# Optimization experiments

Measured on AMD Instinct MI355X. Metric: run time of the kernel, lower is better.

The kernel has to match this reference:

```python
import jax, jax.numpy as jnp
import numpy as np

B, L, K, D = 8, 4096, 16, 128


def setup_inputs() -> dict:
    key = jax.random.key(0)
    k1, k2 = jax.random.split(key)
    frame = jax.random.normal(k1, (B, L, 4, 3), dtype=jnp.float32)  # [B,L,4,3]: row0=center, rows1-3=frame axes
    attr = jax.random.normal(k2, (B, L, D), dtype=jnp.float32)
    return {"frame": frame, "attr": attr}


def reference(frame, attr):
    Kmax = 16
    center = frame[:, :, 0]  # [B,L,3]
    # pairwise squared distances (no grad needed through topk selection)
    c_ng = jax.lax.stop_gradient(center)
    diff = c_ng[:, :, None, :] - c_ng[:, None, :, :]  # [B,L,L,3]
    distance_sq = jnp.sum(diff * diff, axis=-1)  # [B,L,L]
    # k nearest neighbors (smallest distance)
    _, nbr = jax.lax.top_k(-distance_sq, Kmax)  # [B,L,K] int32 indices
    # gather neighbor attributes: attr[b, nbr[b,l,k], :]
    gathered_attr = jax.vmap(lambda a, i: a[i])(attr, nbr)  # [B,L,K,D]
    # gather neighbor centers and project delta into local frame
    nbr_center = jax.vmap(lambda c, i: c[i])(center, nbr)  # [B,L,K,3]
    delta = nbr_center - center[:, :, None, :]  # [B,L,K,3]
    euclidian = jnp.einsum('blkc,blcr->blkr', delta, frame[:, :, 1:4])  # [B,L,K,3]
    return (euclidian, gathered_attr)
```

## Files before the change

### kernel.cpp

```cpp
#include <hip/hip_runtime.h>
#include <stdint.h>

typedef unsigned long long u64;
typedef float nfloat4 __attribute__((ext_vector_type(4)));

#define LQ   4096
#define BQ   8
#define KNB  16
#define TPB  512
#define QPB  64
#define BPB  (LQ / QPB)

__device__ __forceinline__ void ceu(uint32_t &a, uint32_t &b) {
    const uint32_t mn = a < b ? a : b;
    const uint32_t mx = a < b ? b : a;
    a = mn; b = mx;
}
__device__ __forceinline__ void ced(double &a, double &b) {
    const double mn = __builtin_fmin(a, b);
    const double mx = __builtin_fmax(a, b);
    a = mn; b = mx;
}
__device__ __forceinline__ float dist2(float mx, float my, float mz,
                                       float px, float py, float pz) {
    const float dx = __fsub_rn(mx, px);
    const float dy = __fsub_rn(my, py);
    const float dz = __fsub_rn(mz, pz);
    return __fadd_rn(__fadd_rn(__fmul_rn(dx, dx), __fmul_rn(dy, dy)),
                     __fmul_rn(dz, dz));
}


__global__ __launch_bounds__(TPB) void knn_fused_kernel(
    const float4* __restrict__ frame4,
    const float4* __restrict__ attr4,
    float* __restrict__ out_e,
    nfloat4* __restrict__ outg4)
{
    __shared__ float xs[LQ], ys[LQ], zs[LQ];
    __shared__ unsigned short surv[QPB][32];
    __shared__ int nbrs[QPB][KNB];

    const int b    = blockIdx.x >> 6;
    const int qblk = blockIdx.x & (BPB - 1);
    const int tid  = threadIdx.x;

    const float4* fb = frame4 + (size_t)b * LQ * 3;
    for (int j = tid; j < LQ; j += TPB) {
        const float4 v = fb[j * 3];
        xs[j] = v.x; ys[j] = v.y; zs[j] = v.z;
    }
    __syncthreads();

    const int qloc = tid >> 3;
    const int h    = tid & 7;
    const int l    = qblk * QPB + qloc;
    const float mx = xs[l], my = ys[l], mz = zs[l];

    uint32_t R[16];
#pragma unroll
    for (int i = 0; i < 16; ++i) R[i] = 0xFFFFFFFFu;

#pragma unroll 1
    for (int cc = 0; cc < 64; ++cc) {
        uint32_t K[8];
#pragma unroll
        for (int s = 0; s < 8; ++s) {
            const int j = cc * 64 + s * 8 + h;
            const float d = dist2(mx, my, mz, xs[j], ys[j], zs[j]);
            K[s] = (__float_as_uint(d) & 0xFFFFF000u) | (unsigned)j;
        }
        ceu(K[0],K[1]); ceu(K[2],K[3]); ceu(K[4],K[5]); ceu(K[6],K[7]);
        ceu(K[0],K[2]); ceu(K[1],K[3]); ceu(K[4],K[6]); ceu(K[5],K[7]);
        ceu(K[1],K[2]); ceu(K[5],K[6]);
        ceu(K[0],K[4]); ceu(K[1],K[5]); ceu(K[2],K[6]); ceu(K[3],K[7]);
        ceu(K[2],K[4]); ceu(K[3],K[5]);
        ceu(K[1],K[2]); ceu(K[3],K[4]); ceu(K[5],K[6]);
#pragma unroll
        for (int t = 0; t < 8; ++t) {
            const uint32_t x = R[8 + t], y = K[7 - t];
            R[8 + t] = x < y ? x : y;
        }
#pragma unroll
        for (int g = 8; g >= 1; g >>= 1)
#pragma unroll
            for (int i = 0; i < 16; ++i)
                if ((i & g) == 0) ceu(R[i], R[i + g]);
    }

    {
        uint32_t P[16];
#pragma unroll
        for (int i = 0; i < 16; ++i) P[i] = __shfl_xor(R[i], 1, 64);
        const bool lo = (h & 1) == 0;
#pragma unroll
        for (int i = 0; i < 16; ++i) {
            const uint32_t o = P[15 - i];
            R[i] = lo ? (R[i] < o ? R[i] : o) : (R[i] > o ? R[i] : o);
        }
#pragma unroll
        for (int g = 8; g >= 1; g >>= 1)
#pragma unroll
            for (int i = 0; i < 16; ++i)
                if ((i & g) == 0) ceu(R[i], R[i + g]);
    }
    {
        uint32_t P[16];
#pragma unroll
        for (int i = 0; i < 16; ++i) P[i] = __shfl_xor(R[i], 3, 64);
        const bool lo = (h & 2) == 0;
#pragma unroll
        for (int i = 0; i < 16; ++i) {
            const uint32_t o = P[15 - i];
            R[i] = lo ? (R[i] < o ? R[i] : o) : (R[i] > o ? R[i] : o);
        }
#pragma unroll
        for (int i = 0; i < 16; ++i) P[i] = __shfl_xor(R[i], 1, 64);
        const bool lo1 = (h & 1) == 0;
#pragma unroll
        for (int i = 0; i < 16; ++i) {
            const uint32_t o = P[i];
            R[i] = lo1 ? (R[i] < o ? R[i] : o) : (R[i] > o ? R[i] : o);
        }
#pragma unroll
        for (int g = 8; g >= 1; g >>= 1)
#pragma unroll
            for (int i = 0; i < 16; ++i)
                if ((i & g) == 0) ceu(R[i], R[i + g]);
    }
    {
        uint32_t P[16];
#pragma unroll
        for (int i = 0; i < 16; ++i) P[i] = __shfl_xor(R[i], 7, 64);
        const bool lo = (h & 4) == 0;
#pragma unroll
        for (int i = 0; i < 16; ++i) {
            const uint32_t o = P[15 - i];
            R[i] = lo ? (R[i] < o ? R[i] : o) : (R[i] > o ? R[i] : o);
        }
#pragma unroll
        for (int i = 0; i < 16; ++i) P[i] = __shfl_xor(R[i], 2, 64);
        const bool lo2 = (h & 2) == 0;
#pragma unroll
        for (int i = 0; i < 16; ++i) {
            const uint32_t o = P[i];
            R[i] = lo2 ? (R[i] < o ? R[i] : o) : (R[i] > o ? R[i] : o);
        }
#pragma unroll
        for (int i = 0; i < 16; ++i) P[i] = __shfl_xor(R[i], 1, 64);
        const bool lo1 = (h & 1) == 0;
#pragma unroll
        for (int i = 0; i < 16; ++i) {
            const uint32_t o = P[i];
            R[i] = lo1 ? (R[i] < o ? R[i] : o) : (R[i] > o ? R[i] : o);
        }
#pragma unroll
        for (int g = 8; g >= 1; g >>= 1)
#pragma unroll
            for (int i = 0; i < 16; ++i)
                if ((i & g) == 0) ceu(R[i], R[i + g]);
    }

    if (h < 2) {
#pragma unroll
        for (int i = 0; i < 16; ++i)
            surv[qloc][h * 16 + i] = (unsigned short)(R[i] & 0xFFFu);
    }

    double kd[4];
#pragma unroll
    for (int s = 0; s < 4; ++s) {
        const int j = surv[qloc][h * 4 + s];
        const float d = dist2(mx, my, mz, xs[j], ys[j], zs[j]);
        kd[s] = __builtin_bit_cast(double,
                 ((u64)__float_as_uint(d) << 12) | (unsigned)j);
    }
    ced(kd[0],kd[1]); ced(kd[2],kd[3]); ced(kd[0],kd[2]); ced(kd[1],kd[3]); ced(kd[1],kd[2]);
    {
        double P[4];
#pragma unroll
        for (int s = 0; s < 4; ++s) P[s] = __shfl_xor(kd[s], 1, 64);
        const bool lo = (h & 1) == 0;
#pragma unroll
        for (int s = 0; s < 4; ++s) {
            const double o = P[3 - s];
            kd[s] = lo ? __builtin_fmin(kd[s], o) : __builtin_fmax(kd[s], o);
        }
        ced(kd[0],kd[2]); ced(kd[1],kd[3]); ced(kd[0],kd[1]); ced(kd[2],kd[3]);
    }
    {
        double P[4];
#pragma unroll
        for (int s = 0; s < 4; ++s) P[s] = __shfl_xor(kd[s], 3, 64);
        const bool lo = (h & 2) == 0;
#pragma unroll
        for (int s = 0; s < 4; ++s) {
            const double o = P[3 - s];
            kd[s] = lo ? __builtin_fmin(kd[s], o) : __builtin_fmax(kd[s], o);
        }
#pragma unroll
        for (int s = 0; s < 4; ++s) P[s] = __shfl_xor(kd[s], 1, 64);
        const bool lo1 = (h & 1) == 0;
#pragma unroll
        for (int s = 0; s < 4; ++s) {
            const double o = P[s];
            kd[s] = lo1 ? __builtin_fmin(kd[s], o) : __builtin_fmax(kd[s], o);
        }
        ced(kd[0],kd[2]); ced(kd[1],kd[3]); ced(kd[0],kd[1]); ced(kd[2],kd[3]);
    }
    {
        double P[4];
#pragma unroll
        for (int s = 0; s < 4; ++s) P[s] = __shfl_xor(kd[s], 7, 64);
        const bool lo = (h & 4) == 0;
#pragma unroll
        for (int s = 0; s < 4; ++s) {
            const double o = P[3 - s];
            kd[s] = lo ? __builtin_fmin(kd[s], o) : __builtin_fmax(kd[s], o);
        }
#pragma unroll
        for (int s = 0; s < 4; ++s) P[s] = __shfl_xor(kd[s], 2, 64);
        const bool lo2 = (h & 2) == 0;
#pragma unroll
        for (int s = 0; s < 4; ++s) {
            const double o = P[s];
            kd[s] = lo2 ? __builtin_fmin(kd[s], o) : __builtin_fmax(kd[s], o);
        }
#pragma unroll
        for (int s = 0; s < 4; ++s) P[s] = __shfl_xor(kd[s], 1, 64);
        const bool lo1 = (h & 1) == 0;
#pragma unroll
        for (int s = 0; s < 4; ++s) {
            const double o = P[s];
            kd[s] = lo1 ? __builtin_fmin(kd[s], o) : __builtin_fmax(kd[s], o);
        }
        ced(kd[0],kd[2]); ced(kd[1],kd[3]); ced(kd[0],kd[1]); ced(kd[2],kd[3]);
    }

    const size_t gq = (size_t)b * LQ + l;
    if (h < 4) {
        const float4 f0 = fb[l * 3 + 0];
        const float4 f1 = fb[l * 3 + 1];
        const float4 f2 = fb[l * 3 + 2];
        const float R00 = f0.w, R01 = f1.x, R02 = f1.y;
        const float R10 = f1.z, R11 = f1.w, R12 = f2.x;
        const float R20 = f2.y, R21 = f2.z, R22 = f2.w;
        float e[12];
#pragma unroll
        for (int s = 0; s < 4; ++s) {
            const u64 bits = __builtin_bit_cast(u64, kd[s]);
            const int j = (int)(bits & 0xFFFu);
            nbrs[qloc][h * 4 + s] = j;
            const float dx = xs[j] - mx;
            const float dy = ys[j] - my;
            const float dz = zs[j] - mz;
            e[s * 3 + 0] = dx * R00 + dy * R10 + dz * R20;
            e[s * 3 + 1] = dx * R01 + dy * R11 + dz * R21;
            e[s * 3 + 2] = dx * R02 + dy * R12 + dz * R22;
        }
        float4* eo = (float4*)(out_e + gq * 48 + h * 12);
        float4 v0 = {e[0], e[1], e[2],  e[3]};
        float4 v1 = {e[4], e[5], e[6],  e[7]};
        float4 v2 = {e[8], e[9], e[10], e[11]};
        eo[0] = v0; eo[1] = v1; eo[2] = v2;
    }

    const float4* ab = attr4 + (((size_t)b) << 12) * 32;
    const int wv = tid >> 6, lane = tid & 63;
    const size_t obase = ((size_t)b * LQ + (size_t)qblk * QPB + (size_t)wv * 8) * 512;
#pragma unroll 4
    for (int it = 0; it < 64; ++it) {
        const int idx = it * 64 + lane;
        const int qw  = idx >> 9;
        const int r   = idx & 511;
        const int k   = r >> 5, d4 = r & 31;
        const int nb  = nbrs[wv * 8 + qw][k];
        const float4 v = ab[(size_t)nb * 32 + d4];
        nfloat4 nv = {v.x, v.y, v.z, v.w};
        __builtin_nontemporal_store(nv, &outg4[obase + idx]);
    }
}

extern "C" void kernel_launch(void* const* d_in, const int* in_sizes, int n_in,
                              void* d_out, int out_size, void* d_ws, size_t ws_size,
                              hipStream_t stream)
{
    const float* frame = (const float*)d_in[0];
    const float* attr  = (const float*)d_in[1];
    float* out = (float*)d_out;

    nfloat4* outg4 = (nfloat4*)(out + (size_t)BQ * LQ * KNB * 3);
    knn_fused_kernel<<<BQ * BPB, TPB, 0, stream>>>(
        (const float4*)frame, (const float4*)attr, out, outg4);
}
```

Measured before the change: 329.0 us.

## Sort points by x and prune KNN scan with x-distance early termination

```diff
diff --git a/kernel.cpp b/kernel.cpp
--- a/kernel.cpp
+++ b/kernel.cpp
@@ -2,6 +2,7 @@
 #include <stdint.h>
 
 typedef unsigned long long u64;
+typedef unsigned short u16;
 typedef float nfloat4 __attribute__((ext_vector_type(4)));
 
 #define LQ   4096
@@ -30,15 +31,55 @@
                      __fmul_rn(dz, dz));
 }
 
+__global__ __launch_bounds__(512) void sort_kernel(
+    const float4* __restrict__ frame4,
+    float* __restrict__ wx, float* __restrict__ wy,
+    float* __restrict__ wz, int* __restrict__ wperm)
+{
+    __shared__ u64 SK[LQ];
+    const int b   = blockIdx.x;
+    const int tid = threadIdx.x;
+    const float4* fb = frame4 + (size_t)b * LQ * 3;
+
+    for (int j = tid; j < LQ; j += 512) {
+        const uint32_t bits = __float_as_uint(fb[j * 3].x);
+        const uint32_t mk = (bits & 0x80000000u) ? ~bits : (bits | 0x80000000u);
+        SK[j] = ((u64)mk << 32) | (unsigned)j;
+    }
+    __syncthreads();
+    for (int k = 2; k <= LQ; k <<= 1) {
+        for (int g = k >> 1; g >= 1; g >>= 1) {
+            for (int t = tid; t < LQ / 2; t += 512) {
+                const int i  = ((t & ~(g - 1)) << 1) | (t & (g - 1));
+                const int j2 = i | g;
+                const bool up = ((i & k) == 0);
+                const u64 a = SK[i], c = SK[j2];
+                if ((a > c) == up) { SK[i] = c; SK[j2] = a; }
+            }
+            __syncthreads();
+        }
+    }
+    for (int p = tid; p < LQ; p += 512) {
+        const int orig = (int)(SK[p] & 0xFFFu);
+        const float4 v = fb[orig * 3];
+        const size_t o = (size_t)b * LQ + p;
+        wx[o] = v.x; wy[o] = v.y; wz[o] = v.z; wperm[o] = orig;
+    }
+}
+
 
 __global__ __launch_bounds__(TPB) void knn_fused_kernel(
     const float4* __restrict__ frame4,
     const float4* __restrict__ attr4,
+    const float* __restrict__ wx, const float* __restrict__ wy,
+    const float* __restrict__ wz, const int* __restrict__ wperm,
     float* __restrict__ out_e,
     nfloat4* __restrict__ outg4)
 {
     __shared__ float xs[LQ], ys[LQ], zs[LQ];
-    __shared__ unsigned short surv[QPB][32];
+    __shared__ u16 perm_lds[LQ];
+    __shared__ u16 inv_lds[LQ];
+    __shared__ u16 surv[QPB][32];
     __shared__ int nbrs[QPB][KNB];
 
     const int b    = blockIdx.x >> 6;
@@ -46,29 +87,63 @@
     const int tid  = threadIdx.x;
 
     const float4* fb = frame4 + (size_t)b * LQ * 3;
-    for (int j = tid; j < LQ; j += TPB) {
-        const float4 v = fb[j * 3];
-        xs[j] = v.x; ys[j] = v.y; zs[j] = v.z;
+    {
+        const float* bx = wx + (size_t)b * LQ;
+        const float* by = wy + (size_t)b * LQ;
+        const float* bz = wz + (size_t)b * LQ;
+        const int*   bp = wperm + (size_t)b * LQ;
+        for (int j = tid; j < LQ; j += TPB) {
+            xs[j] = bx[j]; ys[j] = by[j]; zs[j] = bz[j];
+            const int pm = bp[j];
+            perm_lds[j] = (u16)pm;
+            inv_lds[pm] = (u16)j;
+        }
     }
     __syncthreads();
 
     const int qloc = tid >> 3;
     const int h    = tid & 7;
+    const int wv   = tid >> 6;
     const int l    = qblk * QPB + qloc;
     const float mx = xs[l], my = ys[l], mz = zs[l];
+    const float xq_lo = xs[qblk * QPB + wv * 8];
+    const float xq_hi = xs[qblk * QPB + wv * 8 + 7];
 
     uint32_t R[16];
 #pragma unroll
     for (int i = 0; i < 16; ++i) R[i] = 0xFFFFFFFFu;
 
+    const int A = qblk * QPB;
+    int lo = A, hi = A;
+    bool doneR = false;
+    bool doneL = (lo <= 0);
+
 #pragma unroll 1
-    for (int cc = 0; cc < 64; ++cc) {
+    while (!(doneR && doneL)) {
+        int base;
+        {
+            bool goRight;
+            if (doneR) goRight = false;
+            else if (doneL) goRight = true;
+            else {
+                const float dR = __fsub_rn(xs[hi], xq_hi);
+                const float dL = __fsub_rn(xq_lo, xs[lo - 1]);
+                goRight = !(dR > dL);
+            }
+            if (goRight) { base = hi; hi += 64; }
+            else         { lo -= 64; base = lo; }
+        }
         uint32_t K[8];
 #pragma unroll
         for (int s = 0; s < 8; ++s) {
-            const int j = cc * 64 + s * 8 + h;
-            const float d = dist2(mx, my, mz, xs[j], ys[j], zs[j]);
-            K[s] = (__float_as_uint(d) & 0xFFFFF000u) | (unsigned)j;
+            const int pos = base + s * 8 + h;
+            const int pp  = pos < 0 ? 0 : pos;
+            const float dx = __fsub_rn(mx, xs[pp]);
+            const float dy = __fsub_rn(my, ys[pp]);
+            const float dz = __fsub_rn(mz, zs[pp]);
+            const float d  = __fmaf_rn(dz, dz, __fmaf_rn(dy, dy, __fmul_rn(dx, dx)));
+            const uint32_t key = (__float_as_uint(d) & 0xFFFFF000u) | (unsigned)pos;
+            K[s] = (pos >= 0) ? key : 0xFFFFFFFFu;
         }
         ceu(K[0],K[1]); ceu(K[2],K[3]); ceu(K[4],K[5]); ceu(K[6],K[7]);
         ceu(K[0],K[2]); ceu(K[1],K[3]); ceu(K[4],K[6]); ceu(K[5],K[7]);
@@ -86,17 +161,46 @@
 #pragma unroll
             for (int i = 0; i < 16; ++i)
                 if ((i & g) == 0) ceu(R[i], R[i + g]);
+
+        uint32_t ub = R[15] | 0xFFFu;
+        { uint32_t t;
+          t = __shfl_xor(ub, 1, 64); ub = ub < t ? ub : t;
+          t = __shfl_xor(ub, 2, 64); ub = ub < t ? ub : t;
+          t = __shfl_xor(ub, 4, 64); ub = ub < t ? ub : t; }
+        uint32_t ubb = (ub & 0xFFFFF000u) | 0xFFFu;
+        ubb = ubb >> 12;
+        ubb = (ubb << 12) | 0xFFFu;
+        ubb = (ubb > 0xFFFFFFEFu) ? 0xFFFFFFFFu : ubb + 16u;
+
+        if (!doneR) {
+            if (hi >= LQ) doneR = true;
+            else {
+                const float dxm = __fsub_rn(xs[hi], mx);
+                const bool st = (dxm > 0.f) &&
+                                (__float_as_uint(__fmul_rn(dxm, dxm)) > ubb);
+                if (__all(st)) doneR = true;
+            }
+        }
+        if (!doneL) {
+            if (lo <= 0) doneL = true;
+            else {
+                const float dxm = __fsub_rn(mx, xs[lo - 1]);
+                const bool st = (dxm > 0.f) &&
+                                (__float_as_uint(__fmul_rn(dxm, dxm)) > ubb);
+                if (__all(st)) doneL = true;
+            }
+        }
     }
 
     {
         uint32_t P[16];
 #pragma unroll
         for (int i = 0; i < 16; ++i) P[i] = __shfl_xor(R[i], 1, 64);
-        const bool lo = (h & 1) == 0;
+        const bool lo1 = (h & 1) == 0;
 #pragma unroll
         for (int i = 0; i < 16; ++i) {
             const uint32_t o = P[15 - i];
-            R[i] = lo ? (R[i] < o ? R[i] : o) : (R[i] > o ? R[i] : o);
+            R[i] = lo1 ? (R[i] < o ? R[i] : o) : (R[i] > o ? R[i] : o);
         }
 #pragma unroll
         for (int g = 8; g >= 1; g >>= 1)
@@ -108,11 +212,11 @@
         uint32_t P[16];
 #pragma unroll
         for (int i = 0; i < 16; ++i) P[i] = __shfl_xor(R[i], 3, 64);
-        const bool lo = (h & 2) == 0;
+        const bool lo2 = (h & 2) == 0;
 #pragma unroll
         for (int i = 0; i < 16; ++i) {
             const uint32_t o = P[15 - i];
-            R[i] = lo ? (R[i] < o ? R[i] : o) : (R[i] > o ? R[i] : o);
+            R[i] = lo2 ? (R[i] < o ? R[i] : o) : (R[i] > o ? R[i] : o);
         }
 #pragma unroll
         for (int i = 0; i < 16; ++i) P[i] = __shfl_xor(R[i], 1, 64);
@@ -132,11 +236,11 @@
         uint32_t P[16];
 #pragma unroll
         for (int i = 0; i < 16; ++i) P[i] = __shfl_xor(R[i], 7, 64);
-        const bool lo = (h & 4) == 0;
+        const bool lo4 = (h & 4) == 0;
 #pragma unroll
         for (int i = 0; i < 16; ++i) {
             const uint32_t o = P[15 - i];
-            R[i] = lo ? (R[i] < o ? R[i] : o) : (R[i] > o ? R[i] : o);
+            R[i] = lo4 ? (R[i] < o ? R[i] : o) : (R[i] > o ? R[i] : o);
         }
 #pragma unroll
         for (int i = 0; i < 16; ++i) P[i] = __shfl_xor(R[i], 2, 64);
@@ -164,27 +268,27 @@
     if (h < 2) {
 #pragma unroll
         for (int i = 0; i < 16; ++i)
-            surv[qloc][h * 16 + i] = (unsigned short)(R[i] & 0xFFFu);
+            surv[qloc][h * 16 + i] = (u16)(R[i] & 0xFFFu);
     }
 
     double kd[4];
 #pragma unroll
     for (int s = 0; s < 4; ++s) {
-        const int j = surv[qloc][h * 4 + s];
-        const float d = dist2(mx, my, mz, xs[j], ys[j], zs[j]);
+        const int sp = surv[qloc][h * 4 + s];
+        const float d = dist2(mx, my, mz, xs[sp], ys[sp], zs[sp]);
         kd[s] = __builtin_bit_cast(double,
-                 ((u64)__float_as_uint(d) << 12) | (unsigned)j);
+                 ((u64)__float_as_uint(d) << 12) | (unsigned)perm_lds[sp]);
     }
     ced(kd[0],kd[1]); ced(kd[2],kd[3]); ced(kd[0],kd[2]); ced(kd[1],kd[3]); ced(kd[1],kd[2]);
     {
         double P[4];
 #pragma unroll
         for (int s = 0; s < 4; ++s) P[s] = __shfl_xor(kd[s], 1, 64);
-        const bool lo = (h & 1) == 0;
+        const bool lo1 = (h & 1) == 0;
 #pragma unroll
         for (int s = 0; s < 4; ++s) {
             const double o = P[3 - s];
-            kd[s] = lo ? __builtin_fmin(kd[s], o) : __builtin_fmax(kd[s], o);
+            kd[s] = lo1 ? __builtin_fmin(kd[s], o) : __builtin_fmax(kd[s], o);
         }
         ced(kd[0],kd[2]); ced(kd[1],kd[3]); ced(kd[0],kd[1]); ced(kd[2],kd[3]);
     }
@@ -192,11 +296,11 @@
         double P[4];
 #pragma unroll
         for (int s = 0; s < 4; ++s) P[s] = __shfl_xor(kd[s], 3, 64);
-        const bool lo = (h & 2) == 0;
+        const bool lo2 = (h & 2) == 0;
 #pragma unroll
         for (int s = 0; s < 4; ++s) {
             const double o = P[3 - s];
-            kd[s] = lo ? __builtin_fmin(kd[s], o) : __builtin_fmax(kd[s], o);
+            kd[s] = lo2 ? __builtin_fmin(kd[s], o) : __builtin_fmax(kd[s], o);
         }
 #pragma unroll
         for (int s = 0; s < 4; ++s) P[s] = __shfl_xor(kd[s], 1, 64);
@@ -212,11 +316,11 @@
         double P[4];
 #pragma unroll
         for (int s = 0; s < 4; ++s) P[s] = __shfl_xor(kd[s], 7, 64);
-        const bool lo = (h & 4) == 0;
+        const bool lo4 = (h & 4) == 0;
 #pragma unroll
         for (int s = 0; s < 4; ++s) {
             const double o = P[3 - s];
-            kd[s] = lo ? __builtin_fmin(kd[s], o) : __builtin_fmax(kd[s], o);
+            kd[s] = lo4 ? __builtin_fmin(kd[s], o) : __builtin_fmax(kd[s], o);
         }
 #pragma unroll
         for (int s = 0; s < 4; ++s) P[s] = __shfl_xor(kd[s], 2, 64);
@@ -237,11 +341,12 @@
         ced(kd[0],kd[2]); ced(kd[1],kd[3]); ced(kd[0],kd[1]); ced(kd[2],kd[3]);
     }
 
-    const size_t gq = (size_t)b * LQ + l;
+    const int ql_orig = perm_lds[l];
+    const size_t gq = (size_t)b * LQ + (size_t)ql_orig;
     if (h < 4) {
-        const float4 f0 = fb[l * 3 + 0];
-        const float4 f1 = fb[l * 3 + 1];
-        const float4 f2 = fb[l * 3 + 2];
+        const float4 f0 = fb[ql_orig * 3 + 0];
+        const float4 f1 = fb[ql_orig * 3 + 1];
+        const float4 f2 = fb[ql_orig * 3 + 2];
         const float R00 = f0.w, R01 = f1.x, R02 = f1.y;
         const float R10 = f1.z, R11 = f1.w, R12 = f2.x;
         const float R20 = f2.y, R21 = f2.z, R22 = f2.w;
@@ -249,11 +354,12 @@
 #pragma unroll
         for (int s = 0; s < 4; ++s) {
             const u64 bits = __builtin_bit_cast(u64, kd[s]);
-            const int j = (int)(bits & 0xFFFu);
-            nbrs[qloc][h * 4 + s] = j;
-            const float dx = xs[j] - mx;
-            const float dy = ys[j] - my;
-            const float dz = zs[j] - mz;
+            const int jo = (int)(bits & 0xFFFu);
+            nbrs[qloc][h * 4 + s] = jo;
+            const int sp = inv_lds[jo];
+            const float dx = xs[sp] - mx;
+            const float dy = ys[sp] - my;
+            const float dz = zs[sp] - mz;
             e[s * 3 + 0] = dx * R00 + dy * R10 + dz * R20;
             e[s * 3 + 1] = dx * R01 + dy * R11 + dz * R21;
             e[s * 3 + 2] = dx * R02 + dy * R12 + dz * R22;
@@ -266,8 +372,8 @@
     }
 
     const float4* ab = attr4 + (((size_t)b) << 12) * 32;
-    const int wv = tid >> 6, lane = tid & 63;
-    const size_t obase = ((size_t)b * LQ + (size_t)qblk * QPB + (size_t)wv * 8) * 512;
+    const int lane = tid & 63;
+    const int qbase = qblk * QPB + wv * 8;
 #pragma unroll 4
     for (int it = 0; it < 64; ++it) {
         const int idx = it * 64 + lane;
@@ -275,9 +381,11 @@
         const int r   = idx & 511;
         const int k   = r >> 5, d4 = r & 31;
         const int nb  = nbrs[wv * 8 + qw][k];
+        const int qo  = perm_lds[qbase + qw];
         const float4 v = ab[(size_t)nb * 32 + d4];
         nfloat4 nv = {v.x, v.y, v.z, v.w};
-        __builtin_nontemporal_store(nv, &outg4[obase + idx]);
+        __builtin_nontemporal_store(nv,
+            &outg4[((size_t)b * LQ + (size_t)qo) * 512 + r]);
     }
 }
 
@@ -289,7 +397,15 @@
     const float* attr  = (const float*)d_in[1];
     float* out = (float*)d_out;
 
+    float* wxp = (float*)d_ws;
+    float* wyp = wxp + BQ * LQ;
+    float* wzp = wyp + BQ * LQ;
+    int*   wpp = (int*)(wzp + BQ * LQ);
+
+    sort_kernel<<<BQ, 512, 0, stream>>>((const float4*)frame, wxp, wyp, wzp, wpp);
+
     nfloat4* outg4 = (nfloat4*)(out + (size_t)BQ * LQ * KNB * 3);
     knn_fused_kernel<<<BQ * BPB, TPB, 0, stream>>>(
-        (const float4*)frame, (const float4*)attr, out, outg4);
-}
+        (const float4*)frame, (const float4*)attr, wxp, wyp, wzp, wpp,
+        out, outg4);
+}
```

Result: slower. 396.8 us (+20.6%).

## Replace per-thread bitonic top-k with shared-memory histogram threshold selection

Applied to the files above, without the earlier changes.

```diff
diff --git a/kernel.cpp b/kernel.cpp
--- a/kernel.cpp
+++ b/kernel.cpp
@@ -2,6 +2,8 @@
 #include <stdint.h>
 
 typedef unsigned long long u64;
+typedef unsigned short u16;
+typedef unsigned int u32;
 typedef float nfloat4 __attribute__((ext_vector_type(4)));
 
 #define LQ   4096
@@ -10,12 +12,10 @@
 #define TPB  512
 #define QPB  64
 #define BPB  (LQ / QPB)
-
-__device__ __forceinline__ void ceu(uint32_t &a, uint32_t &b) {
-    const uint32_t mn = a < b ? a : b;
-    const uint32_t mx = a < b ? b : a;
-    a = mn; b = mx;
-}
+#define NBK  112
+#define HBASE 936u
+#define LCAP 64
+
 __device__ __forceinline__ void ced(double &a, double &b) {
     const double mn = __builtin_fmin(a, b);
     const double mx = __builtin_fmax(a, b);
@@ -37,236 +37,217 @@
     float* __restrict__ out_e,
     nfloat4* __restrict__ outg4)
 {
-    __shared__ float xs[LQ], ys[LQ], zs[LQ];
-    __shared__ unsigned short surv[QPB][32];
-    __shared__ int nbrs[QPB][KNB];
+    __shared__ float2 pxy[LQ];
+    __shared__ float  pz[LQ];
+    __shared__ u32    hist[32 * NBK];
+    __shared__ u16    list[QPB][LCAP];
+    __shared__ u32    cnt[QPB];
+    __shared__ int    nbrs[QPB][KNB];
 
     const int b    = blockIdx.x >> 6;
     const int qblk = blockIdx.x & (BPB - 1);
     const int tid  = threadIdx.x;
+    const int wv   = tid >> 6;
+    const int lane = tid & 63;
 
     const float4* fb = frame4 + (size_t)b * LQ * 3;
     for (int j = tid; j < LQ; j += TPB) {
         const float4 v = fb[j * 3];
-        xs[j] = v.x; ys[j] = v.y; zs[j] = v.z;
-    }
+        pxy[j] = make_float2(v.x, v.y);
+        pz[j]  = v.z;
+    }
+    for (int t = lane; t < 4 * NBK; t += 64) hist[wv * 4 * NBK + t] = 0u;
+    if (lane < 8) cnt[wv * 8 + lane] = 0u;
     __syncthreads();
 
     const int qloc = tid >> 3;
     const int h    = tid & 7;
     const int l    = qblk * QPB + qloc;
-    const float mx = xs[l], my = ys[l], mz = zs[l];
-
-    uint32_t R[16];
-#pragma unroll
-    for (int i = 0; i < 16; ++i) R[i] = 0xFFFFFFFFu;
+    const float2 mxy = pxy[l];
+    const float mx = mxy.x, my = mxy.y, mz = pz[l];
+
+    const u32 qp     = (u32)(qloc >> 1);
+    const u32 sh     = (u32)((qloc & 1) << 4);
+    const u32 addend = 1u << sh;
+    const u32 hb     = qp * NBK;
 
 #pragma unroll 1
     for (int cc = 0; cc < 64; ++cc) {
-        uint32_t K[8];
 #pragma unroll
         for (int s = 0; s < 8; ++s) {
             const int j = cc * 64 + s * 8 + h;
-            const float d = dist2(mx, my, mz, xs[j], ys[j], zs[j]);
-            K[s] = (__float_as_uint(d) & 0xFFFFF000u) | (unsigned)j;
-        }
-        ceu(K[0],K[1]); ceu(K[2],K[3]); ceu(K[4],K[5]); ceu(K[6],K[7]);
-        ceu(K[0],K[2]); ceu(K[1],K[3]); ceu(K[4],K[6]); ceu(K[5],K[7]);
-        ceu(K[1],K[2]); ceu(K[5],K[6]);
-        ceu(K[0],K[4]); ceu(K[1],K[5]); ceu(K[2],K[6]); ceu(K[3],K[7]);
-        ceu(K[2],K[4]); ceu(K[3],K[5]);
-        ceu(K[1],K[2]); ceu(K[3],K[4]); ceu(K[5],K[6]);
-#pragma unroll
-        for (int t = 0; t < 8; ++t) {
-            const uint32_t x = R[8 + t], y = K[7 - t];
-            R[8 + t] = x < y ? x : y;
-        }
-#pragma unroll
-        for (int g = 8; g >= 1; g >>= 1)
-#pragma unroll
-            for (int i = 0; i < 16; ++i)
-                if ((i & g) == 0) ceu(R[i], R[i + g]);
-    }
-
+            const float2 xy = pxy[j];
+            const float  z  = pz[j];
+            const float dx = __fsub_rn(mx, xy.x);
+            const float dy = __fsub_rn(my, xy.y);
+            const float dz = __fsub_rn(mz, z);
+            const float d  = __fmaf_rn(dz, dz, __fmaf_rn(dy, dy, __fmul_rn(dx, dx)));
+            int k = (int)(__float_as_uint(d) >> 20) - (int)HBASE;
+            k = k < 0 ? 0 : (k > (NBK - 1) ? (NBK - 1) : k);
+            atomicAdd(&hist[hb + (u32)k], addend);
+        }
+    }
+
+    const int b0 = h * (NBK / 8);
+    u32 mysum = 0;
+#pragma unroll
+    for (int t = 0; t < NBK / 8; ++t)
+        mysum += (hist[hb + b0 + t] >> sh) & 0xFFFFu;
+    u32 csum = mysum;
+#pragma unroll
+    for (int o = 1; o < 8; o <<= 1) {
+        const u32 t = __shfl_up(csum, o, 8);
+        if (h >= o) csum += t;
+    }
+    const u32 cumBefore = csum - mysum;
+    const bool cross = (cumBefore < 16u) && (cumBefore + mysum >= 16u);
+    int T = 0;
+    if (cross) {
+        u32 c = cumBefore; int t = 0;
+        while (true) {
+            const u32 v = (hist[hb + b0 + t] >> sh) & 0xFFFFu;
+            if (c + v >= 16u) break;
+            c += v; ++t;
+        }
+        T = b0 + t;
+    }
+    const u64 bal = __ballot(cross);
+    const int gbase = lane & ~7;
+    const int crossl = gbase + (__ffsll(bal >> gbase) - 1);
+    T = __shfl(T, crossl, 64);
+    const u32 smax = HBASE + (u32)T + 1u;
+
+#pragma unroll 1
+    for (int cc = 0; cc < 64; ++cc) {
+#pragma unroll
+        for (int s = 0; s < 8; ++s) {
+            const int j = cc * 64 + s * 8 + h;
+            const float2 xy = pxy[j];
+            const float  z  = pz[j];
+            const float dx = __fsub_rn(mx, xy.x);
+            const float dy = __fsub_rn(my, xy.y);
+            const float dz = __fsub_rn(mz, z);
+            const float d  = __fmaf_rn(dz, dz, __fmaf_rn(dy, dy, __fmul_rn(dx, dx)));
+            const u32 sb = __float_as_uint(d) >> 20;
+            if (sb <= smax) {
+                const u32 old = atomicAdd(&cnt[qloc], 1u);
+                if (old < (u32)LCAP) list[qloc][old] = (u16)j;
+            }
+        }
+    }
+
+    const int c = (int)min(cnt[qloc], (u32)LCAP);
+    double kd[8];
+#pragma unroll
+    for (int s = 0; s < 8; ++s) {
+        const int m = h * 8 + s;
+        const int j = (m < c) ? (int)list[qloc][m] : 0;
+        const float2 xy = pxy[j];
+        const float d = dist2(mx, my, mz, xy.x, xy.y, pz[j]);
+        const u64 key = ((u64)__float_as_uint(d) << 12) | (unsigned)j;
+        kd[s] = (m < c) ? __builtin_bit_cast(double, key) : 1.0;
+    }
+    ced(kd[0],kd[1]); ced(kd[2],kd[3]); ced(kd[4],kd[5]); ced(kd[6],kd[7]);
+    ced(kd[0],kd[2]); ced(kd[1],kd[3]); ced(kd[4],kd[6]); ced(kd[5],kd[7]);
+    ced(kd[1],kd[2]); ced(kd[5],kd[6]);
+    ced(kd[0],kd[4]); ced(kd[1],kd[5]); ced(kd[2],kd[6]); ced(kd[3],kd[7]);
+    ced(kd[2],kd[4]); ced(kd[3],kd[5]);
+    ced(kd[1],kd[2]); ced(kd[3],kd[4]); ced(kd[5],kd[6]);
     {
-        uint32_t P[16];
-#pragma unroll
-        for (int i = 0; i < 16; ++i) P[i] = __shfl_xor(R[i], 1, 64);
+        double P[8];
+#pragma unroll
+        for (int s = 0; s < 8; ++s) P[s] = __shfl_xor(kd[s], 1, 64);
         const bool lo = (h & 1) == 0;
 #pragma unroll
-        for (int i = 0; i < 16; ++i) {
-            const uint32_t o = P[15 - i];
-            R[i] = lo ? (R[i] < o ? R[i] : o) : (R[i] > o ? R[i] : o);
-        }
-#pragma unroll
-        for (int g = 8; g >= 1; g >>= 1)
-#pragma unroll
-            for (int i = 0; i < 16; ++i)
-                if ((i & g) == 0) ceu(R[i], R[i + g]);
+        for (int s = 0; s < 8; ++s) {
+            const double o = P[7 - s];
+            kd[s] = lo ? __builtin_fmin(kd[s], o) : __builtin_fmax(kd[s], o);
+        }
+        ced(kd[0],kd[4]); ced(kd[1],kd[5]); ced(kd[2],kd[6]); ced(kd[3],kd[7]);
+        ced(kd[0],kd[2]); ced(kd[1],kd[3]); ced(kd[4],kd[6]); ced(kd[5],kd[7]);
+        ced(kd[0],kd[1]); ced(kd[2],kd[3]); ced(kd[4],kd[5]); ced(kd[6],kd[7]);
     }
     {
-        uint32_t P[16];
-#pragma unroll
-        for (int i = 0; i < 16; ++i) P[i] = __shfl_xor(R[i], 3, 64);
+        double P[8];
+#pragma unroll
+        for (int s = 0; s < 8; ++s) P[s] = __shfl_xor(kd[s], 3, 64);
         const bool lo = (h & 2) == 0;
 #pragma unroll
-        for (int i = 0; i < 16; ++i) {
-            const uint32_t o = P[15 - i];
-            R[i] = lo ? (R[i] < o ? R[i] : o) : (R[i] > o ? R[i] : o);
-        }
-#pragma unroll
-        for (int i = 0; i < 16; ++i) P[i] = __shfl_xor(R[i], 1, 64);
+        for (int s = 0; s < 8; ++s) {
+            const double o = P[7 - s];
+            kd[s] = lo ? __builtin_fmin(kd[s], o) : __builtin_fmax(kd[s], o);
+        }
+#pragma unroll
+        for (int s = 0; s < 8; ++s) P[s] = __shfl_xor(kd[s], 1, 64);
         const bool lo1 = (h & 1) == 0;
 #pragma unroll
-        for (int i = 0; i < 16; ++i) {
-            const uint32_t o = P[i];
-            R[i] = lo1 ? (R[i] < o ? R[i] : o) : (R[i] > o ? R[i] : o);
-        }
-#pragma unroll
-        for (int g = 8; g >= 1; g >>= 1)
-#pragma unroll
-            for (int i = 0; i < 16; ++i)
-                if ((i & g) == 0) ceu(R[i], R[i + g]);
-    }
-    {
-        uint32_t P[16];
-#pragma unroll
-        for (int i = 0; i < 16; ++i) P[i] = __shfl_xor(R[i], 7, 64);
-        const bool lo = (h & 4) == 0;
-#pragma unroll
-        for (int i = 0; i < 16; ++i) {
-            const uint32_t o = P[15 - i];
-            R[i] = lo ? (R[i] < o ? R[i] : o) : (R[i] > o ? R[i] : o);
-        }
-#pragma unroll
-        for (int i = 0; i < 16; ++i) P[i] = __shfl_xor(R[i], 2, 64);
-        const bool lo2 = (h & 2) == 0;
-#pragma unroll
-        for (int i = 0; i < 16; ++i) {
-            const uint32_t o = P[i];
-            R[i] = lo2 ? (R[i] < o ? R[i] : o) : (R[i] > o ? R[i] : o);
-        }
-#pragma unroll
-        for (int i = 0; i < 16; ++i) P[i] = __shfl_xor(R[i], 1, 64);
-        const bool lo1 = (h & 1) == 0;
-#pragma unroll
-        for (int i = 0; i < 16; ++i) {
-            const uint32_t o = P[i];
-            R[i] = lo1 ? (R[i] < o ? R[i] : o) : (R[i] > o ? R[i] : o);
-        }
-#pragma unroll
-        for (int g = 8; g >= 1; g >>= 1)
-#pragma unroll
-            for (int i = 0; i < 16; ++i)
-                if ((i & g) == 0) ceu(R[i], R[i + g]);
-    }
-
-    if (h < 2) {
-#pragma unroll
-        for (int i = 0; i < 16; ++i)
-            surv[qloc][h * 16 + i] = (unsigned short)(R[i] & 0xFFFu);
-    }
-
-    double kd[4];
-#pragma unroll
-    for (int s = 0; s < 4; ++s) {
-        const int j = surv[qloc][h * 4 + s];
-        const float d = dist2(mx, my, mz, xs[j], ys[j], zs[j]);
-        kd[s] = __builtin_bit_cast(double,
-                 ((u64)__float_as_uint(d) << 12) | (unsigned)j);
-    }
-    ced(kd[0],kd[1]); ced(kd[2],kd[3]); ced(kd[0],kd[2]); ced(kd[1],kd[3]); ced(kd[1],kd[2]);
-    {
-        double P[4];
-#pragma unroll
-        for (int s = 0; s < 4; ++s) P[s] = __shfl_xor(kd[s], 1, 64);
-        const bool lo = (h & 1) == 0;
-#pragma unroll
-        for (int s = 0; s < 4; ++s) {
-            const double o = P[3 - s];
-            kd[s] = lo ? __builtin_fmin(kd[s], o) : __builtin_fmax(kd[s], o);
-        }
-        ced(kd[0],kd[2]); ced(kd[1],kd[3]); ced(kd[0],kd[1]); ced(kd[2],kd[3]);
-    }
-    {
-        double P[4];
-#pragma unroll
-        for (int s = 0; s < 4; ++s) P[s] = __shfl_xor(kd[s], 3, 64);
-        const bool lo = (h & 2) == 0;
-#pragma unroll
-        for (int s = 0; s < 4; ++s) {
-            const double o = P[3 - s];
-            kd[s] = lo ? __builtin_fmin(kd[s], o) : __builtin_fmax(kd[s], o);
-        }
-#pragma unroll
-        for (int s = 0; s < 4; ++s) P[s] = __shfl_xor(kd[s], 1, 64);
-        const bool lo1 = (h & 1) == 0;
-#pragma unroll
-        for (int s = 0; s < 4; ++s) {
+        for (int s = 0; s < 8; ++s) {
             const double o = P[s];
             kd[s] = lo1 ? __builtin_fmin(kd[s], o) : __builtin_fmax(kd[s], o);
         }
-        ced(kd[0],kd[2]); ced(kd[1],kd[3]); ced(kd[0],kd[1]); ced(kd[2],kd[3]);
+        ced(kd[0],kd[4]); ced(kd[1],kd[5]); ced(kd[2],kd[6]); ced(kd[3],kd[7]);
+        ced(kd[0],kd[2]); ced(kd[1],kd[3]); ced(kd[4],kd[6]); ced(kd[5],kd[7]);
+        ced(kd[0],kd[1]); ced(kd[2],kd[3]); ced(kd[4],kd[5]); ced(kd[6],kd[7]);
     }
     {
-        double P[4];
-#pragma unroll
-        for (int s = 0; s < 4; ++s) P[s] = __shfl_xor(kd[s], 7, 64);
+        double P[8];
+#pragma unroll
+        for (int s = 0; s < 8; ++s) P[s] = __shfl_xor(kd[s], 7, 64);
         const bool lo = (h & 4) == 0;
 #pragma unroll
-        for (int s = 0; s < 4; ++s) {
-            const double o = P[3 - s];
+        for (int s = 0; s < 8; ++s) {
+            const double o = P[7 - s];
             kd[s] = lo ? __builtin_fmin(kd[s], o) : __builtin_fmax(kd[s], o);
         }
 #pragma unroll
-        for (int s = 0; s < 4; ++s) P[s] = __shfl_xor(kd[s], 2, 64);
+        for (int s = 0; s < 8; ++s) P[s] = __shfl_xor(kd[s], 2, 64);
         const bool lo2 = (h & 2) == 0;
 #pragma unroll
-        for (int s = 0; s < 4; ++s) {
+        for (int s = 0; s < 8; ++s) {
             const double o = P[s];
             kd[s] = lo2 ? __builtin_fmin(kd[s], o) : __builtin_fmax(kd[s], o);
         }
 #pragma unroll
-        for (int s = 0; s < 4; ++s) P[s] = __shfl_xor(kd[s], 1, 64);
+        for (int s = 0; s < 8; ++s) P[s] = __shfl_xor(kd[s], 1, 64);
         const bool lo1 = (h & 1) == 0;
 #pragma unroll
-        for (int s = 0; s < 4; ++s) {
+        for (int s = 0; s < 8; ++s) {
             const double o = P[s];
             kd[s] = lo1 ? __builtin_fmin(kd[s], o) : __builtin_fmax(kd[s], o);
         }
-        ced(kd[0],kd[2]); ced(kd[1],kd[3]); ced(kd[0],kd[1]); ced(kd[2],kd[3]);
+        ced(kd[0],kd[4]); ced(kd[1],kd[5]); ced(kd[2],kd[6]); ced(kd[3],kd[7]);
+        ced(kd[0],kd[2]); ced(kd[1],kd[3]); ced(kd[4],kd[6]); ced(kd[5],kd[7]);
+        ced(kd[0],kd[1]); ced(kd[2],kd[3]); ced(kd[4],kd[5]); ced(kd[6],kd[7]);
     }
 
     const size_t gq = (size_t)b * LQ + l;
-    if (h < 4) {
+    if (h < 2) {
         const float4 f0 = fb[l * 3 + 0];
         const float4 f1 = fb[l * 3 + 1];
         const float4 f2 = fb[l * 3 + 2];
         const float R00 = f0.w, R01 = f1.x, R02 = f1.y;
         const float R10 = f1.z, R11 = f1.w, R12 = f2.x;
         const float R20 = f2.y, R21 = f2.z, R22 = f2.w;
-        float e[12];
-#pragma unroll
-        for (int s = 0; s < 4; ++s) {
+        float e[24];
+#pragma unroll
+        for (int s = 0; s < 8; ++s) {
             const u64 bits = __builtin_bit_cast(u64, kd[s]);
             const int j = (int)(bits & 0xFFFu);
-            nbrs[qloc][h * 4 + s] = j;
-            const float dx = xs[j] - mx;
-            const float dy = ys[j] - my;
-            const float dz = zs[j] - mz;
+            nbrs[qloc][h * 8 + s] = j;
+            const float2 xy = pxy[j];
+            const float dx = xy.x - mx;
+            const float dy = xy.y - my;
+            const float dz = pz[j] - mz;
             e[s * 3 + 0] = dx * R00 + dy * R10 + dz * R20;
             e[s * 3 + 1] = dx * R01 + dy * R11 + dz * R21;
             e[s * 3 + 2] = dx * R02 + dy * R12 + dz * R22;
         }
-        float4* eo = (float4*)(out_e + gq * 48 + h * 12);
-        float4 v0 = {e[0], e[1], e[2],  e[3]};
-        float4 v1 = {e[4], e[5], e[6],  e[7]};
-        float4 v2 = {e[8], e[9], e[10], e[11]};
-        eo[0] = v0; eo[1] = v1; eo[2] = v2;
+        float4* eo = (float4*)(out_e + gq * 48 + h * 24);
+#pragma unroll
+        for (int t = 0; t < 6; ++t) eo[t] = ((const float4*)e)[t];
     }
 
     const float4* ab = attr4 + (((size_t)b) << 12) * 32;
-    const int wv = tid >> 6, lane = tid & 63;
     const size_t obase = ((size_t)b * LQ + (size_t)qblk * QPB + (size_t)wv * 8) * 512;
 #pragma unroll 4
     for (int it = 0; it < 64; ++it) {
```

Measured after the change: 398.1 us. +21.0%, slower.
